# Optimization experiments

Hardware: AMD Instinct MI355X
Metric: run time of the kernel (lower is better)

## Reference

```python
import jax, jax.numpy as jnp
import numpy as np

B, N, D = 8, 2048, 512

def setup_inputs() -> dict:
    key = jax.random.key(0)
    ks = jax.random.split(key, 8)
    s = 1.0 / np.sqrt(D)
    return {
        "inputs": jax.random.normal(ks[0], (B, N, D), dtype=jnp.float32),
        "mask": jnp.ones((B, N), dtype=jnp.int32),
        "Wk": jax.random.normal(ks[1], (D, D), dtype=jnp.float32) * s,
        "bk": jax.random.normal(ks[2], (D,), dtype=jnp.float32) * s,
        "Wq": jax.random.normal(ks[3], (D, D), dtype=jnp.float32) * s,
        "bq": jax.random.normal(ks[4], (D,), dtype=jnp.float32) * s,
        "Wv": jax.random.normal(ks[5], (D, D), dtype=jnp.float32) * s,
        "bv": jax.random.normal(ks[6], (D,), dtype=jnp.float32) * s,
    }

def reference(inputs, mask, Wk, bk, Wq, bq, Wv, bv):
    # torch Linear: y = x @ W.T + b
    keys = jnp.einsum('bnd,ed->bne', inputs, Wk) + bk
    queries = jnp.einsum('bnd,ed->bne', inputs, Wq) + bq
    values = jnp.einsum('bnd,ed->bne', inputs, Wv) + bv
    norm = jnp.sqrt(jnp.asarray(D, inputs.dtype))
    scores = jnp.einsum('bqd,bkd->bqk', queries, keys) / norm  # [B,N,N]
    scores = jnp.where(mask[:, None, :] == 0, jnp.asarray(-1e9, scores.dtype), scores)
    attn = jax.nn.softmax(scores, axis=-1)
    return jnp.einsum('bqk,bkd->bqd', attn, values)
```

## Files before the change

### kernel.cpp

```cpp
#include <hip/hip_runtime.h>
#include <hip/hip_bf16.h>


typedef __attribute__((ext_vector_type(8))) short short8;
typedef __attribute__((ext_vector_type(4))) float f32x4;

#define DEV __device__ __forceinline__
#define GLOBAL_AS __attribute__((address_space(1)))
#define LDS_AS __attribute__((address_space(3)))

static DEV ushort f2bs(float f) {
  union { float f; unsigned u; } x; x.f = f;
  unsigned r = (x.u + 0x7fffu + ((x.u >> 16) & 1u)) >> 16;
  return (ushort)r;
}

static DEV f32x4 mfma16(short8 a, short8 b, f32x4 c) {
  return __builtin_amdgcn_mfma_f32_16x16x32_bf16(a, b, c, 0, 0, 0);
}

static DEV void async16(const void* g, void* l) {
  __builtin_amdgcn_global_load_lds((const GLOBAL_AS void*)g, (LDS_AS void*)l, 16, 0, 0);
}

__global__ void convert_all(const float* __restrict__ wq, const float* __restrict__ wk,
                            const float* __restrict__ wv, const float* __restrict__ x,
                            ushort* __restrict__ wb, ushort* __restrict__ xb,
                            float* __restrict__ lde) {
  int i = blockIdx.x * 256 + threadIdx.x;
  if (i >= 2293760) {
    int off = (i - 2293760) * 4;
    float4 z; z.x = 0.f; z.y = 0.f; z.z = 0.f; z.w = 0.f;
    *(float4*)(lde + off) = z;
    return;
  }
  const float* src;
  ushort* dst;
  if (i < 196608) {
    int which = i >> 16;
    int off = (i & 65535) * 4;
    src = ((which == 0) ? wq : (which == 1) ? wk : wv) + off;
    dst = wb + (size_t)which * 262144 + off;
  } else {
    int off = (i - 196608) * 4;
    src = x + off;
    dst = xb + off;
  }
  float4 v = *(const float4*)src;
  ushort4 o;
  o.x = f2bs(v.x); o.y = f2bs(v.y); o.z = f2bs(v.z); o.w = f2bs(v.w);
  *(ushort4*)dst = o;
}

#define KLOOP_STAGE(Aptr, lda, Bptr, ldb)                                      \
  do {                                                                         \
    _Pragma("unroll")                                                          \
    for (int t = 0; t < 8; t++) {                                              \
      int rowbase = (t & 3) * 32 + wave * 8;                                   \
      int r = rowbase + (lane >> 3);                                           \
      int gc = (lane & 7) ^ (r & 7);                                           \
      if (t < 4)                                                               \
        async16((Aptr) + (size_t)(rowblk * 128 + r) * (lda) + kb + gc * 8,     \
                &As[rowbase * 64]);                                            \
      else                                                                     \
        async16((Bptr) + (size_t)(colblk * 128 + r) * (ldb) + kb + gc * 8,     \
                &Bs[rowbase * 64]);                                            \
    }                                                                          \
  } while (0)

#define KLOOP_MFMA()                                                           \
  do {                                                                         \
    _Pragma("unroll")                                                          \
    for (int ks = 0; ks < 2; ks++) {                                           \
      short8 af[4], bfr[4];                                                    \
      _Pragma("unroll")                                                        \
      for (int t = 0; t < 4; t++) {                                            \
        int ra = wm * 64 + t * 16 + c16;                                       \
        int rb = wn * 64 + t * 16 + c16;                                       \
        af[t]  = *(const short8*)&As[ra * 64 + (((ks * 4 + quad) ^ (ra & 7)) * 8)]; \
        bfr[t] = *(const short8*)&Bs[rb * 64 + (((ks * 4 + quad) ^ (rb & 7)) * 8)]; \
      }                                                                        \
      _Pragma("unroll")                                                        \
      for (int mt = 0; mt < 4; mt++)                                           \
        _Pragma("unroll")                                                      \
        for (int nt = 0; nt < 4; nt++)                                         \
          acc[mt][nt] = mfma16(af[mt], bfr[nt], acc[mt][nt]);                  \
    }                                                                          \
  } while (0)

__launch_bounds__(256, 4)
__global__ void qkv_gemm(const ushort* __restrict__ Xb, const ushort* __restrict__ Wb,
                         const float* __restrict__ bq, const float* __restrict__ bk,
                         const float* __restrict__ bv,
                         ushort* __restrict__ Qb, ushort* __restrict__ Kb,
                         ushort* __restrict__ Vtb) {
  const int rowblk = blockIdx.x;
  const int colblk = blockIdx.y;
  const int z = colblk >> 2;

  __shared__ ushort S[2 * 128 * 64];
  ushort* As = S;
  ushort* Bs = S + 128 * 64;

  const int tid = threadIdx.x;
  const int wave = tid >> 6, lane = tid & 63, quad = lane >> 4, c16 = lane & 15;
  const int wm = wave & 1, wn = wave >> 1;

  f32x4 acc[4][4];
#pragma unroll
  for (int mt = 0; mt < 4; mt++)
#pragma unroll
    for (int nt = 0; nt < 4; nt++) acc[mt][nt] = (f32x4)0.0f;

  for (int kb = 0; kb < 512; kb += 64) {
    __syncthreads();
    KLOOP_STAGE(Xb, 512, Wb, 512);
    __syncthreads();
    KLOOP_MFMA();
  }

  const float* bias = (z == 0) ? bq : (z == 1) ? bk : bv;
  float bvals[4];
#pragma unroll
  for (int nt = 0; nt < 4; nt++) {
    int eg = colblk * 128 + wn * 64 + nt * 16 + c16;
    bvals[nt] = bias[eg & 511];
  }
  const float sc = (z == 0) ? 0.044194173824159216f : 1.0f;

  const int row0 = rowblk * 128 + wm * 64;
  const int col0 = colblk * 128 + wn * 64;
  if (z < 2) {
    ushort* O = (z == 0) ? Qb : Kb;
#pragma unroll
    for (int mt = 0; mt < 4; mt++)
#pragma unroll
      for (int nt = 0; nt < 4; nt++) {
        int el = (col0 + nt * 16 + c16) & 511;
#pragma unroll
        for (int r = 0; r < 4; r++) {
          int n = row0 + mt * 16 + quad * 4 + r;
          O[(size_t)n * 512 + el] = f2bs((acc[mt][nt][r] + bvals[nt]) * sc);
        }
      }
  } else {
    __syncthreads();
    ushort* T = S;
#pragma unroll
    for (int nt = 0; nt < 4; nt++) {
      int ell = wn * 64 + nt * 16 + c16;
#pragma unroll
      for (int mt = 0; mt < 4; mt++) {
        int n0l = wm * 64 + mt * 16 + quad * 4;
        ushort4 o;
        o.x = f2bs(acc[mt][nt][0] + bvals[nt]);
        o.y = f2bs(acc[mt][nt][1] + bvals[nt]);
        o.z = f2bs(acc[mt][nt][2] + bvals[nt]);
        o.w = f2bs(acc[mt][nt][3] + bvals[nt]);
        *(ushort4*)&T[ell * 128 + (((n0l >> 3) ^ (ell & 15)) << 3) + (n0l & 4)] = o;
      }
    }
    __syncthreads();
    const int c4 = tid & 3, er = tid >> 2;
    const int bb = rowblk >> 4;
    const int nbase = (rowblk & 15) * 128;
    const int elbase = (colblk & 3) * 128;
#pragma unroll
    for (int part = 0; part < 2; part++) {
      int ell = part * 64 + er;
      size_t ge = ((size_t)bb * 512 + elbase + ell) * 2048;
#pragma unroll
      for (int j2 = 0; j2 < 4; j2++) {
        int n0 = j2 * 32 + c4 * 8;
        short8 v = *(short8*)&T[ell * 128 + (((n0 >> 3) ^ (ell & 15)) << 3)];
        *(short8*)(Vtb + ge + nbase + n0) = v;
      }
    }
  }
}

__launch_bounds__(256, 4)
__global__ void gemm_s(const ushort* __restrict__ Kb, const ushort* __restrict__ Qb,
                       const int* __restrict__ mask, ushort* __restrict__ Pm,
                       float* __restrict__ l) {
  const int b = blockIdx.z;
  const int rowblk = blockIdx.x;
  const int colblk = blockIdx.y;
  const ushort* A  = Kb + (size_t)b * 2048 * 512;
  const ushort* Bq = Qb + (size_t)b * 2048 * 512;

  __shared__ ushort S[2 * 128 * 64];
  ushort* As = S;
  ushort* Bs = S + 128 * 64;

  const int tid = threadIdx.x;
  const int wave = tid >> 6, lane = tid & 63, quad = lane >> 4, c16 = lane & 15;
  const int wm = wave & 1, wn = wave >> 1;

  f32x4 acc[4][4];
#pragma unroll
  for (int mt = 0; mt < 4; mt++)
#pragma unroll
    for (int nt = 0; nt < 4; nt++) acc[mt][nt] = (f32x4)0.0f;

  for (int kb = 0; kb < 512; kb += 64) {
    __syncthreads();
    KLOOP_STAGE(A, 512, Bq, 512);
    __syncthreads();
    KLOOP_MFMA();
  }

  const int row0 = rowblk * 128 + wm * 64;
  const int col0 = colblk * 128 + wn * 64;
  float lpart[4] = {0.0f, 0.0f, 0.0f, 0.0f};

  __syncthreads();
  ushort* T = S;
#pragma unroll
  for (int mt = 0; mt < 4; mt++) {
    int key0 = row0 + mt * 16 + quad * 4;
    int k0l  = wm * 64 + mt * 16 + quad * 4;
    int4 mv = *(const int4*)&mask[b * 2048 + key0];
    float mf0 = mv.x ? 1.0f : 0.0f, mf1 = mv.y ? 1.0f : 0.0f;
    float mf2 = mv.z ? 1.0f : 0.0f, mf3 = mv.w ? 1.0f : 0.0f;
#pragma unroll
    for (int nt = 0; nt < 4; nt++) {
      int ql = wn * 64 + nt * 16 + c16;
      float p0 = __expf(acc[mt][nt][0]) * mf0;
      float p1 = __expf(acc[mt][nt][1]) * mf1;
      float p2 = __expf(acc[mt][nt][2]) * mf2;
      float p3 = __expf(acc[mt][nt][3]) * mf3;
      ushort4 o;
      o.x = f2bs(p0); o.y = f2bs(p1); o.z = f2bs(p2); o.w = f2bs(p3);
      *(ushort4*)&T[ql * 128 + (((k0l >> 3) ^ (ql & 15)) << 3) + (k0l & 4)] = o;
      lpart[nt] += p0 + p1 + p2 + p3;
    }
  }
#pragma unroll
  for (int nt = 0; nt < 4; nt++) {
    float v = lpart[nt];
    v += __shfl_xor(v, 16, 64);
    v += __shfl_xor(v, 32, 64);
    if (quad == 0) atomicAdd(&l[b * 2048 + col0 + nt * 16 + c16], v);
  }
  __syncthreads();
  {
    const int c4 = tid & 3, er = tid >> 2;
#pragma unroll
    for (int part = 0; part < 2; part++) {
      int ql = part * 64 + er;
      size_t gq = ((size_t)b * 2048 + colblk * 128 + ql) * 2048;
#pragma unroll
      for (int j2 = 0; j2 < 4; j2++) {
        int n0 = j2 * 32 + c4 * 8;
        short8 v = *(short8*)&T[ql * 128 + (((n0 >> 3) ^ (ql & 15)) << 3)];
        *(short8*)(Pm + gq + rowblk * 128 + n0) = v;
      }
    }
  }
}

__launch_bounds__(256, 4)
__global__ void gemm_o(const ushort* __restrict__ Pm, const ushort* __restrict__ Vtb,
                       const float* __restrict__ l, float* __restrict__ out) {
  const int b = blockIdx.z;
  const int rowblk = blockIdx.x;
  const int colblk = blockIdx.y;
  const ushort* A  = Pm  + (size_t)b * 2048 * 2048;
  const ushort* Bv = Vtb + (size_t)b * 512 * 2048;

  __shared__ ushort S[2 * 128 * 64];
  ushort* As = S;
  ushort* Bs = S + 128 * 64;

  const int tid = threadIdx.x;
  const int wave = tid >> 6, lane = tid & 63, quad = lane >> 4, c16 = lane & 15;
  const int wm = wave & 1, wn = wave >> 1;

  f32x4 acc[4][4];
#pragma unroll
  for (int mt = 0; mt < 4; mt++)
#pragma unroll
    for (int nt = 0; nt < 4; nt++) acc[mt][nt] = (f32x4)0.0f;

  for (int kb = 0; kb < 2048; kb += 64) {
    __syncthreads();
    KLOOP_STAGE(A, 2048, Bv, 2048);
    __syncthreads();
    KLOOP_MFMA();
  }

  const int row0 = rowblk * 128 + wm * 64;
  const int col0 = colblk * 128 + wn * 64;
  float linv[4][4];
#pragma unroll
  for (int mt = 0; mt < 4; mt++)
#pragma unroll
    for (int r = 0; r < 4; r++)
      linv[mt][r] = 1.0f / l[b * 2048 + row0 + mt * 16 + quad * 4 + r];
#pragma unroll
  for (int mt = 0; mt < 4; mt++)
#pragma unroll
    for (int nt = 0; nt < 4; nt++) {
      int col = col0 + nt * 16 + c16;
#pragma unroll
      for (int r = 0; r < 4; r++) {
        int row = row0 + mt * 16 + quad * 4 + r;
        out[((size_t)b * 2048 + row) * 512 + col] = acc[mt][nt][r] * linv[mt][r];
      }
    }
}

extern "C" void kernel_launch(void* const* d_in, const int* in_sizes, int n_in,
                              void* d_out, int out_size, void* d_ws, size_t ws_size,
                              hipStream_t stream) {
  (void)in_sizes; (void)n_in; (void)out_size; (void)ws_size;
  const float* X    = (const float*)d_in[0];
  const int*   mask = (const int*)d_in[1];
  const float* Wk   = (const float*)d_in[2];
  const float* bk   = (const float*)d_in[3];
  const float* Wq   = (const float*)d_in[4];
  const float* bq   = (const float*)d_in[5];
  const float* Wv   = (const float*)d_in[6];
  const float* bv   = (const float*)d_in[7];
  float* out = (float*)d_out;

  ushort* ws  = (ushort*)d_ws;
  ushort* Pm  = ws;
  ushort* Xb  = ws;
  ushort* Wb  = ws + (size_t)33554432;
  ushort* Qb  = Wb + (size_t)786432;
  ushort* Kb  = Qb + (size_t)8388608;
  ushort* Vtb = Kb + (size_t)8388608;
  float*  lde = (float*)(Vtb + (size_t)8388608);

  convert_all<<<8976, 256, 0, stream>>>(Wq, Wk, Wv, X, Wb, Xb, lde);
  qkv_gemm<<<dim3(128, 12), 256, 0, stream>>>(Xb, Wb, bq, bk, bv, Qb, Kb, Vtb);
  gemm_s<<<dim3(16, 16, 8), 256, 0, stream>>>(Kb, Qb, mask, Pm, lde);
  gemm_o<<<dim3(16, 4, 8), 256, 0, stream>>>(Pm, Vtb, lde, out);
}
```

Baseline: 217.2 us.

## Fuse score and output GEMMs into a single flash-style attention kernel

Replaces the separate score GEMM, which wrote the full bf16 probability matrix to global memory, and the output GEMM with one fused kernel. Each block keeps a 64-query tile resident in LDS and streams K and V tiles, holding exp scores in LDS. Row sums are accumulated in LDS rather than with global atomics, so the zeroing of the global sum buffer goes away. This removes the large Pm write and read, but the grid shrinks to 256 blocks of 512 threads with about 112KB of LDS each. K/V loads are not double-buffered, so occupancy is low and loads are exposed behind syncthreads.

```diff
diff --git a/kernel.cpp b/kernel.cpp
--- a/kernel.cpp
+++ b/kernel.cpp
@@ -25,15 +25,8 @@
 
 __global__ void convert_all(const float* __restrict__ wq, const float* __restrict__ wk,
                             const float* __restrict__ wv, const float* __restrict__ x,
-                            ushort* __restrict__ wb, ushort* __restrict__ xb,
-                            float* __restrict__ lde) {
+                            ushort* __restrict__ wb, ushort* __restrict__ xb) {
   int i = blockIdx.x * 256 + threadIdx.x;
-  if (i >= 2293760) {
-    int off = (i - 2293760) * 4;
-    float4 z; z.x = 0.f; z.y = 0.f; z.z = 0.f; z.w = 0.f;
-    *(float4*)(lde + off) = z;
-    return;
-  }
   const float* src;
   ushort* dst;
   if (i < 196608) {
@@ -179,134 +172,155 @@
   }
 }
 
-__launch_bounds__(256, 4)
-__global__ void gemm_s(const ushort* __restrict__ Kb, const ushort* __restrict__ Qb,
-                       const int* __restrict__ mask, ushort* __restrict__ Pm,
-                       float* __restrict__ l) {
-  const int b = blockIdx.z;
-  const int rowblk = blockIdx.x;
-  const int colblk = blockIdx.y;
-  const ushort* A  = Kb + (size_t)b * 2048 * 512;
-  const ushort* Bq = Qb + (size_t)b * 2048 * 512;
-
-  __shared__ ushort S[2 * 128 * 64];
-  ushort* As = S;
-  ushort* Bs = S + 128 * 64;
+__launch_bounds__(512, 2)
+__global__ void attn_fused(const ushort* __restrict__ Qb, const ushort* __restrict__ Kb,
+                           const ushort* __restrict__ Vtb, const int* __restrict__ mask,
+                           float* __restrict__ out) {
+  const int bid = blockIdx.x;
+  const int b = bid & 7;
+  const int qblk = bid >> 3;
+  const ushort* Qp = Qb + ((size_t)b * 2048 + qblk * 64) * 512;
+  const ushort* Kp = Kb + (size_t)b * 2048 * 512;
+  const ushort* Vp = Vtb + (size_t)b * 512 * 2048;
+
+  extern __shared__ ushort S[];
+  ushort* Qs  = S;
+  ushort* KVs = S + 32768;
+  ushort* Ps  = S + 49152;
+  float*  l_lds = (float*)(S + 57344);
 
   const int tid = threadIdx.x;
   const int wave = tid >> 6, lane = tid & 63, quad = lane >> 4, c16 = lane & 15;
-  const int wm = wave & 1, wn = wave >> 1;
-
-  f32x4 acc[4][4];
-#pragma unroll
-  for (int mt = 0; mt < 4; mt++)
-#pragma unroll
-    for (int nt = 0; nt < 4; nt++) acc[mt][nt] = (f32x4)0.0f;
-
-  for (int kb = 0; kb < 512; kb += 64) {
-    __syncthreads();
-    KLOOP_STAGE(A, 512, Bq, 512);
-    __syncthreads();
-    KLOOP_MFMA();
-  }
-
-  const int row0 = rowblk * 128 + wm * 64;
-  const int col0 = colblk * 128 + wn * 64;
-  float lpart[4] = {0.0f, 0.0f, 0.0f, 0.0f};
-
-  __syncthreads();
-  ushort* T = S;
-#pragma unroll
-  for (int mt = 0; mt < 4; mt++) {
-    int key0 = row0 + mt * 16 + quad * 4;
-    int k0l  = wm * 64 + mt * 16 + quad * 4;
-    int4 mv = *(const int4*)&mask[b * 2048 + key0];
-    float mf0 = mv.x ? 1.0f : 0.0f, mf1 = mv.y ? 1.0f : 0.0f;
-    float mf2 = mv.z ? 1.0f : 0.0f, mf3 = mv.w ? 1.0f : 0.0f;
-#pragma unroll
-    for (int nt = 0; nt < 4; nt++) {
-      int ql = wn * 64 + nt * 16 + c16;
-      float p0 = __expf(acc[mt][nt][0]) * mf0;
-      float p1 = __expf(acc[mt][nt][1]) * mf1;
-      float p2 = __expf(acc[mt][nt][2]) * mf2;
-      float p3 = __expf(acc[mt][nt][3]) * mf3;
-      ushort4 o;
-      o.x = f2bs(p0); o.y = f2bs(p1); o.z = f2bs(p2); o.w = f2bs(p3);
-      *(ushort4*)&T[ql * 128 + (((k0l >> 3) ^ (ql & 15)) << 3) + (k0l & 4)] = o;
-      lpart[nt] += p0 + p1 + p2 + p3;
-    }
-  }
-#pragma unroll
-  for (int nt = 0; nt < 4; nt++) {
+  const int wk = wave & 3, wq = wave >> 2;
+  const int wq2 = wave & 1, wd = wave >> 1;
+
+  if (tid < 64) l_lds[tid] = 0.0f;
+
+#pragma unroll
+  for (int i = 0; i < 8; i++) {
+    int r = wave * 8 + i;
+    int gc = (lane & 48) | ((lane & 15) ^ (r & 15));
+    async16(Qp + (size_t)r * 512 + gc * 8, &Qs[r * 512]);
+  }
+
+  f32x4 acc_o[2][8];
+#pragma unroll
+  for (int mt = 0; mt < 2; mt++)
+#pragma unroll
+    for (int j = 0; j < 8; j++) acc_o[mt][j] = (f32x4)0.0f;
+  float lpart[2] = {0.0f, 0.0f};
+
+  for (int kt = 0; kt < 16; kt++) {
+    const int key0 = kt * 128;
+    f32x4 acc_s[2][2];
+#pragma unroll
+    for (int mt = 0; mt < 2; mt++)
+#pragma unroll
+      for (int nt = 0; nt < 2; nt++) acc_s[mt][nt] = (f32x4)0.0f;
+
+    for (int dc = 0; dc < 4; dc++) {
+      __syncthreads();
+#pragma unroll
+      for (int t = 0; t < 4; t++) {
+        int rowbase = t * 32 + wave * 4;
+        int r = rowbase + (lane >> 4);
+        int gc = (lane & 15) ^ (r & 15);
+        async16(Kp + (size_t)(key0 + r) * 512 + dc * 128 + gc * 8, &KVs[rowbase * 128]);
+      }
+      __syncthreads();
+#pragma unroll
+      for (int ks = 0; ks < 4; ks++) {
+        short8 af[2], qf[2];
+#pragma unroll
+        for (int t = 0; t < 2; t++) {
+          int rk = wk * 32 + t * 16 + c16;
+          af[t] = *(const short8*)&KVs[rk * 128 + (((ks * 4 + quad) ^ (rk & 15)) * 8)];
+          int rq = wq * 32 + t * 16 + c16;
+          int cg = dc * 16 + ks * 4 + quad;
+          qf[t] = *(const short8*)&Qs[rq * 512 + (((cg & 48) | ((cg & 15) ^ (rq & 15))) * 8)];
+        }
+#pragma unroll
+        for (int mt = 0; mt < 2; mt++)
+#pragma unroll
+          for (int nt = 0; nt < 2; nt++)
+            acc_s[mt][nt] = mfma16(af[mt], qf[nt], acc_s[mt][nt]);
+      }
+    }
+
+#pragma unroll
+    for (int mt = 0; mt < 2; mt++) {
+      int k0l = wk * 32 + mt * 16 + quad * 4;
+      int4 mv = *(const int4*)&mask[b * 2048 + key0 + k0l];
+      float mf0 = mv.x ? 1.0f : 0.0f, mf1 = mv.y ? 1.0f : 0.0f;
+      float mf2 = mv.z ? 1.0f : 0.0f, mf3 = mv.w ? 1.0f : 0.0f;
+#pragma unroll
+      for (int nt = 0; nt < 2; nt++) {
+        int ql = wq * 32 + nt * 16 + c16;
+        float p0 = __expf(acc_s[mt][nt][0]) * mf0;
+        float p1 = __expf(acc_s[mt][nt][1]) * mf1;
+        float p2 = __expf(acc_s[mt][nt][2]) * mf2;
+        float p3 = __expf(acc_s[mt][nt][3]) * mf3;
+        ushort4 o;
+        o.x = f2bs(p0); o.y = f2bs(p1); o.z = f2bs(p2); o.w = f2bs(p3);
+        *(ushort4*)&Ps[ql * 128 + (((k0l >> 3) ^ (ql & 15)) << 3) + (k0l & 4)] = o;
+        lpart[nt] += p0 + p1 + p2 + p3;
+      }
+    }
+
+#pragma unroll
+    for (int dv = 0; dv < 4; dv++) {
+      __syncthreads();
+#pragma unroll
+      for (int t = 0; t < 4; t++) {
+        int rowbase = t * 32 + wave * 4;
+        int r = rowbase + (lane >> 4);
+        int gc = (lane & 15) ^ (r & 15);
+        async16(Vp + (size_t)(dv * 128 + r) * 2048 + key0 + gc * 8, &KVs[rowbase * 128]);
+      }
+      __syncthreads();
+#pragma unroll
+      for (int ks = 0; ks < 4; ks++) {
+        short8 ap[2], vf[2];
+#pragma unroll
+        for (int t = 0; t < 2; t++) {
+          int rq = wq2 * 32 + t * 16 + c16;
+          ap[t] = *(const short8*)&Ps[rq * 128 + (((ks * 4 + quad) ^ (rq & 15)) * 8)];
+          int rd = wd * 32 + t * 16 + c16;
+          vf[t] = *(const short8*)&KVs[rd * 128 + (((ks * 4 + quad) ^ (rd & 15)) * 8)];
+        }
+#pragma unroll
+        for (int mt = 0; mt < 2; mt++)
+#pragma unroll
+          for (int nt = 0; nt < 2; nt++)
+            acc_o[mt][dv * 2 + nt] = mfma16(ap[mt], vf[nt], acc_o[mt][dv * 2 + nt]);
+      }
+    }
+  }
+
+#pragma unroll
+  for (int nt = 0; nt < 2; nt++) {
     float v = lpart[nt];
     v += __shfl_xor(v, 16, 64);
     v += __shfl_xor(v, 32, 64);
-    if (quad == 0) atomicAdd(&l[b * 2048 + col0 + nt * 16 + c16], v);
+    if (quad == 0) atomicAdd(&l_lds[wq * 32 + nt * 16 + c16], v);
   }
   __syncthreads();
-  {
-    const int c4 = tid & 3, er = tid >> 2;
-#pragma unroll
-    for (int part = 0; part < 2; part++) {
-      int ql = part * 64 + er;
-      size_t gq = ((size_t)b * 2048 + colblk * 128 + ql) * 2048;
-#pragma unroll
-      for (int j2 = 0; j2 < 4; j2++) {
-        int n0 = j2 * 32 + c4 * 8;
-        short8 v = *(short8*)&T[ql * 128 + (((n0 >> 3) ^ (ql & 15)) << 3)];
-        *(short8*)(Pm + gq + rowblk * 128 + n0) = v;
-      }
-    }
-  }
-}
-
-__launch_bounds__(256, 4)
-__global__ void gemm_o(const ushort* __restrict__ Pm, const ushort* __restrict__ Vtb,
-                       const float* __restrict__ l, float* __restrict__ out) {
-  const int b = blockIdx.z;
-  const int rowblk = blockIdx.x;
-  const int colblk = blockIdx.y;
-  const ushort* A  = Pm  + (size_t)b * 2048 * 2048;
-  const ushort* Bv = Vtb + (size_t)b * 512 * 2048;
-
-  __shared__ ushort S[2 * 128 * 64];
-  ushort* As = S;
-  ushort* Bs = S + 128 * 64;
-
-  const int tid = threadIdx.x;
-  const int wave = tid >> 6, lane = tid & 63, quad = lane >> 4, c16 = lane & 15;
-  const int wm = wave & 1, wn = wave >> 1;
-
-  f32x4 acc[4][4];
-#pragma unroll
-  for (int mt = 0; mt < 4; mt++)
-#pragma unroll
-    for (int nt = 0; nt < 4; nt++) acc[mt][nt] = (f32x4)0.0f;
-
-  for (int kb = 0; kb < 2048; kb += 64) {
-    __syncthreads();
-    KLOOP_STAGE(A, 2048, Bv, 2048);
-    __syncthreads();
-    KLOOP_MFMA();
-  }
-
-  const int row0 = rowblk * 128 + wm * 64;
-  const int col0 = colblk * 128 + wn * 64;
-  float linv[4][4];
-#pragma unroll
-  for (int mt = 0; mt < 4; mt++)
+
+  float linv[2][4];
+#pragma unroll
+  for (int mt = 0; mt < 2; mt++)
 #pragma unroll
     for (int r = 0; r < 4; r++)
-      linv[mt][r] = 1.0f / l[b * 2048 + row0 + mt * 16 + quad * 4 + r];
-#pragma unroll
-  for (int mt = 0; mt < 4; mt++)
-#pragma unroll
-    for (int nt = 0; nt < 4; nt++) {
-      int col = col0 + nt * 16 + c16;
+      linv[mt][r] = 1.0f / l_lds[wq2 * 32 + mt * 16 + quad * 4 + r];
+#pragma unroll
+  for (int mt = 0; mt < 2; mt++)
+#pragma unroll
+    for (int j = 0; j < 8; j++) {
+      int d = (j >> 1) * 128 + wd * 32 + (j & 1) * 16 + c16;
 #pragma unroll
       for (int r = 0; r < 4; r++) {
-        int row = row0 + mt * 16 + quad * 4 + r;
-        out[((size_t)b * 2048 + row) * 512 + col] = acc[mt][nt][r] * linv[mt][r];
+        int row = qblk * 64 + wq2 * 32 + mt * 16 + quad * 4 + r;
+        out[((size_t)b * 2048 + row) * 512 + d] = acc_o[mt][j][r] * linv[mt][r];
       }
     }
 }
@@ -326,16 +340,13 @@
   float* out = (float*)d_out;
 
   ushort* ws  = (ushort*)d_ws;
-  ushort* Pm  = ws;
   ushort* Xb  = ws;
-  ushort* Wb  = ws + (size_t)33554432;
+  ushort* Wb  = Xb + (size_t)8388608;
   ushort* Qb  = Wb + (size_t)786432;
   ushort* Kb  = Qb + (size_t)8388608;
   ushort* Vtb = Kb + (size_t)8388608;
-  float*  lde = (float*)(Vtb + (size_t)8388608);
-
-  convert_all<<<8976, 256, 0, stream>>>(Wq, Wk, Wv, X, Wb, Xb, lde);
+
+  convert_all<<<8960, 256, 0, stream>>>(Wq, Wk, Wv, X, Wb, Xb);
   qkv_gemm<<<dim3(128, 12), 256, 0, stream>>>(Xb, Wb, bq, bk, bv, Qb, Kb, Vtb);
-  gemm_s<<<dim3(16, 16, 8), 256, 0, stream>>>(Kb, Qb, mask, Pm, lde);
-  gemm_o<<<dim3(16, 4, 8), 256, 0, stream>>>(Pm, Vtb, lde, out);
-}
+  attn_fused<<<256, 512, 114944, stream>>>(Qb, Kb, Vtb, mask, out);
+}
```

After: 250.8 us. +15.4%, slower.

## Use 256x256 double-buffered tiles with 512 threads for QKV and score GEMMs

Applied to the files above, without the earlier changes.

Rewrites qkv_gemm and gemm_s to compute 256x256 output tiles with 8 waves, each wave owning 128x64 (32 MFMA accumulators). The K-loop prefetches two stages ahead into a double-buffered 128KB dynamic LDS region with explicit vmcnt waits and barriers, and raises wave priority around the MFMA bursts. This is meant to increase data reuse per loaded byte and overlap global loads with compute. In exchange it uses far more LDS and registers, allows fewer resident blocks, and launches fewer blocks (384 and 512) across the CUs.

```diff
diff --git a/kernel.cpp b/kernel.cpp
--- a/kernel.cpp
+++ b/kernel.cpp
@@ -52,6 +52,229 @@
   *(ushort4*)dst = o;
 }
 
+#define STAGE256(buf, Aptr, lda, Bptr, ldb, kb)                                \
+  do {                                                                         \
+    ushort* bA_ = Sd + (buf) * 32768;                                          \
+    ushort* bB_ = bA_ + 16384;                                                 \
+    _Pragma("unroll")                                                          \
+    for (int st = 0; st < 8; st++) {                                           \
+      int rowbase = (st & 3) * 64 + wave * 8;                                  \
+      int r = rowbase + (lane >> 3);                                           \
+      int gc = (lane & 7) ^ (r & 7);                                           \
+      if (st < 4)                                                              \
+        async16((Aptr) + (size_t)(rowblk * 256 + r) * (lda) + (kb) + gc * 8,   \
+                &bA_[rowbase * 64]);                                           \
+      else                                                                     \
+        async16((Bptr) + (size_t)(colblk * 256 + r) * (ldb) + (kb) + gc * 8,   \
+                &bB_[rowbase * 64]);                                           \
+    }                                                                          \
+  } while (0)
+
+#define COMPUTE256(buf)                                                        \
+  do {                                                                         \
+    const ushort* cA_ = Sd + (buf) * 32768;                                    \
+    const ushort* cB_ = cA_ + 16384;                                           \
+    _Pragma("unroll")                                                          \
+    for (int ks = 0; ks < 2; ks++) {                                           \
+      short8 af[8], bf[4];                                                     \
+      _Pragma("unroll")                                                        \
+      for (int mf = 0; mf < 8; mf++) {                                         \
+        int ra = wm * 128 + mf * 16 + c16;                                     \
+        af[mf] = *(const short8*)&cA_[ra * 64 + (((ks * 4 + quad) ^ (ra & 7)) * 8)]; \
+      }                                                                        \
+      _Pragma("unroll")                                                        \
+      for (int nf = 0; nf < 4; nf++) {                                         \
+        int rb = wn * 64 + nf * 16 + c16;                                      \
+        bf[nf] = *(const short8*)&cB_[rb * 64 + (((ks * 4 + quad) ^ (rb & 7)) * 8)]; \
+      }                                                                        \
+      __builtin_amdgcn_s_setprio(1);                                           \
+      _Pragma("unroll")                                                        \
+      for (int mf = 0; mf < 8; mf++)                                           \
+        _Pragma("unroll")                                                      \
+        for (int nf = 0; nf < 4; nf++)                                         \
+          acc[mf][nf] = mfma16(af[mf], bf[nf], acc[mf][nf]);                   \
+      __builtin_amdgcn_s_setprio(0);                                           \
+    }                                                                          \
+  } while (0)
+
+#define KLOOP256(Aptr, lda, Bptr, ldb, NT)                                     \
+  do {                                                                         \
+    STAGE256(0, Aptr, lda, Bptr, ldb, 0);                                      \
+    STAGE256(1, Aptr, lda, Bptr, ldb, 64);                                     \
+    asm volatile("s_waitcnt vmcnt(8)" ::: "memory");                           \
+    __builtin_amdgcn_sched_barrier(0);                                         \
+    __builtin_amdgcn_s_barrier();                                              \
+    __builtin_amdgcn_sched_barrier(0);                                         \
+    for (int t = 0; t < (NT); t++) {                                           \
+      COMPUTE256(t & 1);                                                       \
+      if (t == (NT) - 1) break;                                                \
+      __builtin_amdgcn_sched_barrier(0);                                       \
+      __builtin_amdgcn_s_barrier();                                            \
+      __builtin_amdgcn_sched_barrier(0);                                       \
+      if (t + 2 < (NT)) {                                                      \
+        STAGE256(t & 1, Aptr, lda, Bptr, ldb, (t + 2) * 64);                   \
+        asm volatile("s_waitcnt vmcnt(8)" ::: "memory");                       \
+      } else {                                                                 \
+        asm volatile("s_waitcnt vmcnt(0)" ::: "memory");                       \
+      }                                                                        \
+      __builtin_amdgcn_sched_barrier(0);                                       \
+      __builtin_amdgcn_s_barrier();                                            \
+      __builtin_amdgcn_sched_barrier(0);                                       \
+    }                                                                          \
+  } while (0)
+
+__launch_bounds__(512, 2)
+__global__ void qkv_gemm(const ushort* __restrict__ Xb, const ushort* __restrict__ Wb,
+                         const float* __restrict__ bq, const float* __restrict__ bk,
+                         const float* __restrict__ bv,
+                         ushort* __restrict__ Qb, ushort* __restrict__ Kb,
+                         ushort* __restrict__ Vtb) {
+  const int rowblk = blockIdx.x;
+  const int colblk = blockIdx.y;
+  const int z = colblk >> 1;
+
+  extern __shared__ ushort Sd[];
+
+  const int tid = threadIdx.x;
+  const int wave = tid >> 6, lane = tid & 63, quad = lane >> 4, c16 = lane & 15;
+  const int wm = wave >> 2, wn = wave & 3;
+
+  f32x4 acc[8][4];
+#pragma unroll
+  for (int mf = 0; mf < 8; mf++)
+#pragma unroll
+    for (int nf = 0; nf < 4; nf++) acc[mf][nf] = (f32x4)0.0f;
+
+  KLOOP256(Xb, 512, Wb, 512, 8);
+
+  const float* bias = (z == 0) ? bq : (z == 1) ? bk : bv;
+  float bvals[4];
+#pragma unroll
+  for (int nf = 0; nf < 4; nf++)
+    bvals[nf] = bias[(colblk & 1) * 256 + wn * 64 + nf * 16 + c16];
+  const float sc = (z == 0) ? 0.044194173824159216f : 1.0f;
+
+  const int row0 = rowblk * 256 + wm * 128;
+  if (z < 2) {
+    ushort* O = (z == 0) ? Qb : Kb;
+#pragma unroll
+    for (int mf = 0; mf < 8; mf++)
+#pragma unroll
+      for (int nf = 0; nf < 4; nf++) {
+        int el = (colblk & 1) * 256 + wn * 64 + nf * 16 + c16;
+#pragma unroll
+        for (int r = 0; r < 4; r++) {
+          int n = row0 + mf * 16 + quad * 4 + r;
+          O[(size_t)n * 512 + el] = f2bs((acc[mf][nf][r] + bvals[nf]) * sc);
+        }
+      }
+  } else {
+    __syncthreads();
+    ushort* T = Sd;
+#pragma unroll
+    for (int nf = 0; nf < 4; nf++) {
+      int ell = wn * 64 + nf * 16 + c16;
+#pragma unroll
+      for (int mf = 0; mf < 8; mf++) {
+        int n0 = wm * 128 + mf * 16 + quad * 4;
+        ushort4 o;
+        o.x = f2bs(acc[mf][nf][0] + bvals[nf]);
+        o.y = f2bs(acc[mf][nf][1] + bvals[nf]);
+        o.z = f2bs(acc[mf][nf][2] + bvals[nf]);
+        o.w = f2bs(acc[mf][nf][3] + bvals[nf]);
+        *(ushort4*)&T[ell * 256 + (((n0 >> 3) ^ (ell & 31)) << 3) + (n0 & 4)] = o;
+      }
+    }
+    __syncthreads();
+    const int b = rowblk >> 3;
+    const int nbase = (rowblk & 7) * 256;
+    const int elbase = (colblk & 1) * 256;
+    const int c4 = tid & 3;
+#pragma unroll
+    for (int outer = 0; outer < 2; outer++) {
+      int er = outer * 128 + (tid >> 2);
+      size_t ge = ((size_t)b * 512 + elbase + er) * 2048;
+#pragma unroll
+      for (int j = 0; j < 8; j++) {
+        int ch = j * 4 + c4;
+        short8 v = *(short8*)&T[er * 256 + ((ch ^ (er & 31)) << 3)];
+        *(short8*)(Vtb + ge + nbase + ch * 8) = v;
+      }
+    }
+  }
+}
+
+__launch_bounds__(512, 2)
+__global__ void gemm_s(const ushort* __restrict__ Kb, const ushort* __restrict__ Qb,
+                       const int* __restrict__ mask, ushort* __restrict__ Pm,
+                       float* __restrict__ l) {
+  const int b = blockIdx.z;
+  const int rowblk = blockIdx.x;
+  const int colblk = blockIdx.y;
+  const ushort* A  = Kb + (size_t)b * 2048 * 512;
+  const ushort* Bq = Qb + (size_t)b * 2048 * 512;
+
+  extern __shared__ ushort Sd[];
+
+  const int tid = threadIdx.x;
+  const int wave = tid >> 6, lane = tid & 63, quad = lane >> 4, c16 = lane & 15;
+  const int wm = wave >> 2, wn = wave & 3;
+
+  f32x4 acc[8][4];
+#pragma unroll
+  for (int mf = 0; mf < 8; mf++)
+#pragma unroll
+    for (int nf = 0; nf < 4; nf++) acc[mf][nf] = (f32x4)0.0f;
+
+  KLOOP256(A, 512, Bq, 512, 8);
+
+  float lpart[4] = {0.0f, 0.0f, 0.0f, 0.0f};
+  __syncthreads();
+  ushort* T = Sd;
+#pragma unroll
+  for (int mf = 0; mf < 8; mf++) {
+    int keyl = wm * 128 + mf * 16 + quad * 4;
+    int4 mv = *(const int4*)&mask[b * 2048 + rowblk * 256 + keyl];
+    float m0 = mv.x ? 1.0f : 0.0f, m1 = mv.y ? 1.0f : 0.0f;
+    float m2 = mv.z ? 1.0f : 0.0f, m3 = mv.w ? 1.0f : 0.0f;
+#pragma unroll
+    for (int nf = 0; nf < 4; nf++) {
+      int ql = wn * 64 + nf * 16 + c16;
+      float p0 = __expf(acc[mf][nf][0]) * m0;
+      float p1 = __expf(acc[mf][nf][1]) * m1;
+      float p2 = __expf(acc[mf][nf][2]) * m2;
+      float p3 = __expf(acc[mf][nf][3]) * m3;
+      ushort4 o;
+      o.x = f2bs(p0); o.y = f2bs(p1); o.z = f2bs(p2); o.w = f2bs(p3);
+      *(ushort4*)&T[ql * 256 + (((keyl >> 3) ^ (ql & 31)) << 3) + (keyl & 4)] = o;
+      lpart[nf] += p0 + p1 + p2 + p3;
+    }
+  }
+#pragma unroll
+  for (int nf = 0; nf < 4; nf++) {
+    float v = lpart[nf];
+    v += __shfl_xor(v, 16, 64);
+    v += __shfl_xor(v, 32, 64);
+    if (quad == 0)
+      atomicAdd(&l[b * 2048 + colblk * 256 + wn * 64 + nf * 16 + c16], v);
+  }
+  __syncthreads();
+  {
+    const int c4 = tid & 3;
+#pragma unroll
+    for (int outer = 0; outer < 2; outer++) {
+      int qr = outer * 128 + (tid >> 2);
+      size_t gq = ((size_t)b * 2048 + colblk * 256 + qr) * 2048;
+#pragma unroll
+      for (int j = 0; j < 8; j++) {
+        int ch = j * 4 + c4;
+        short8 v = *(short8*)&T[qr * 256 + ((ch ^ (qr & 31)) << 3)];
+        *(short8*)(Pm + gq + rowblk * 256 + ch * 8) = v;
+      }
+    }
+  }
+}
+
 #define KLOOP_STAGE(Aptr, lda, Bptr, ldb)                                      \
   do {                                                                         \
     _Pragma("unroll")                                                          \
@@ -87,178 +310,6 @@
           acc[mt][nt] = mfma16(af[mt], bfr[nt], acc[mt][nt]);                  \
     }                                                                          \
   } while (0)
-
-__launch_bounds__(256, 4)
-__global__ void qkv_gemm(const ushort* __restrict__ Xb, const ushort* __restrict__ Wb,
-                         const float* __restrict__ bq, const float* __restrict__ bk,
-                         const float* __restrict__ bv,
-                         ushort* __restrict__ Qb, ushort* __restrict__ Kb,
-                         ushort* __restrict__ Vtb) {
-  const int rowblk = blockIdx.x;
-  const int colblk = blockIdx.y;
-  const int z = colblk >> 2;
-
-  __shared__ ushort S[2 * 128 * 64];
-  ushort* As = S;
-  ushort* Bs = S + 128 * 64;
-
-  const int tid = threadIdx.x;
-  const int wave = tid >> 6, lane = tid & 63, quad = lane >> 4, c16 = lane & 15;
-  const int wm = wave & 1, wn = wave >> 1;
-
-  f32x4 acc[4][4];
-#pragma unroll
-  for (int mt = 0; mt < 4; mt++)
-#pragma unroll
-    for (int nt = 0; nt < 4; nt++) acc[mt][nt] = (f32x4)0.0f;
-
-  for (int kb = 0; kb < 512; kb += 64) {
-    __syncthreads();
-    KLOOP_STAGE(Xb, 512, Wb, 512);
-    __syncthreads();
-    KLOOP_MFMA();
-  }
-
-  const float* bias = (z == 0) ? bq : (z == 1) ? bk : bv;
-  float bvals[4];
-#pragma unroll
-  for (int nt = 0; nt < 4; nt++) {
-    int eg = colblk * 128 + wn * 64 + nt * 16 + c16;
-    bvals[nt] = bias[eg & 511];
-  }
-  const float sc = (z == 0) ? 0.044194173824159216f : 1.0f;
-
-  const int row0 = rowblk * 128 + wm * 64;
-  const int col0 = colblk * 128 + wn * 64;
-  if (z < 2) {
-    ushort* O = (z == 0) ? Qb : Kb;
-#pragma unroll
-    for (int mt = 0; mt < 4; mt++)
-#pragma unroll
-      for (int nt = 0; nt < 4; nt++) {
-        int el = (col0 + nt * 16 + c16) & 511;
-#pragma unroll
-        for (int r = 0; r < 4; r++) {
-          int n = row0 + mt * 16 + quad * 4 + r;
-          O[(size_t)n * 512 + el] = f2bs((acc[mt][nt][r] + bvals[nt]) * sc);
-        }
-      }
-  } else {
-    __syncthreads();
-    ushort* T = S;
-#pragma unroll
-    for (int nt = 0; nt < 4; nt++) {
-      int ell = wn * 64 + nt * 16 + c16;
-#pragma unroll
-      for (int mt = 0; mt < 4; mt++) {
-        int n0l = wm * 64 + mt * 16 + quad * 4;
-        ushort4 o;
-        o.x = f2bs(acc[mt][nt][0] + bvals[nt]);
-        o.y = f2bs(acc[mt][nt][1] + bvals[nt]);
-        o.z = f2bs(acc[mt][nt][2] + bvals[nt]);
-        o.w = f2bs(acc[mt][nt][3] + bvals[nt]);
-        *(ushort4*)&T[ell * 128 + (((n0l >> 3) ^ (ell & 15)) << 3) + (n0l & 4)] = o;
-      }
-    }
-    __syncthreads();
-    const int c4 = tid & 3, er = tid >> 2;
-    const int bb = rowblk >> 4;
-    const int nbase = (rowblk & 15) * 128;
-    const int elbase = (colblk & 3) * 128;
-#pragma unroll
-    for (int part = 0; part < 2; part++) {
-      int ell = part * 64 + er;
-      size_t ge = ((size_t)bb * 512 + elbase + ell) * 2048;
-#pragma unroll
-      for (int j2 = 0; j2 < 4; j2++) {
-        int n0 = j2 * 32 + c4 * 8;
-        short8 v = *(short8*)&T[ell * 128 + (((n0 >> 3) ^ (ell & 15)) << 3)];
-        *(short8*)(Vtb + ge + nbase + n0) = v;
-      }
-    }
-  }
-}
-
-__launch_bounds__(256, 4)
-__global__ void gemm_s(const ushort* __restrict__ Kb, const ushort* __restrict__ Qb,
-                       const int* __restrict__ mask, ushort* __restrict__ Pm,
-                       float* __restrict__ l) {
-  const int b = blockIdx.z;
-  const int rowblk = blockIdx.x;
-  const int colblk = blockIdx.y;
-  const ushort* A  = Kb + (size_t)b * 2048 * 512;
-  const ushort* Bq = Qb + (size_t)b * 2048 * 512;
-
-  __shared__ ushort S[2 * 128 * 64];
-  ushort* As = S;
-  ushort* Bs = S + 128 * 64;
-
-  const int tid = threadIdx.x;
-  const int wave = tid >> 6, lane = tid & 63, quad = lane >> 4, c16 = lane & 15;
-  const int wm = wave & 1, wn = wave >> 1;
-
-  f32x4 acc[4][4];
-#pragma unroll
-  for (int mt = 0; mt < 4; mt++)
-#pragma unroll
-    for (int nt = 0; nt < 4; nt++) acc[mt][nt] = (f32x4)0.0f;
-
-  for (int kb = 0; kb < 512; kb += 64) {
-    __syncthreads();
-    KLOOP_STAGE(A, 512, Bq, 512);
-    __syncthreads();
-    KLOOP_MFMA();
-  }
-
-  const int row0 = rowblk * 128 + wm * 64;
-  const int col0 = colblk * 128 + wn * 64;
-  float lpart[4] = {0.0f, 0.0f, 0.0f, 0.0f};
-
-  __syncthreads();
-  ushort* T = S;
-#pragma unroll
-  for (int mt = 0; mt < 4; mt++) {
-    int key0 = row0 + mt * 16 + quad * 4;
-    int k0l  = wm * 64 + mt * 16 + quad * 4;
-    int4 mv = *(const int4*)&mask[b * 2048 + key0];
-    float mf0 = mv.x ? 1.0f : 0.0f, mf1 = mv.y ? 1.0f : 0.0f;
-    float mf2 = mv.z ? 1.0f : 0.0f, mf3 = mv.w ? 1.0f : 0.0f;
-#pragma unroll
-    for (int nt = 0; nt < 4; nt++) {
-      int ql = wn * 64 + nt * 16 + c16;
-      float p0 = __expf(acc[mt][nt][0]) * mf0;
-      float p1 = __expf(acc[mt][nt][1]) * mf1;
-      float p2 = __expf(acc[mt][nt][2]) * mf2;
-      float p3 = __expf(acc[mt][nt][3]) * mf3;
-      ushort4 o;
-      o.x = f2bs(p0); o.y = f2bs(p1); o.z = f2bs(p2); o.w = f2bs(p3);
-      *(ushort4*)&T[ql * 128 + (((k0l >> 3) ^ (ql & 15)) << 3) + (k0l & 4)] = o;
-      lpart[nt] += p0 + p1 + p2 + p3;
-    }
-  }
-#pragma unroll
-  for (int nt = 0; nt < 4; nt++) {
-    float v = lpart[nt];
-    v += __shfl_xor(v, 16, 64);
-    v += __shfl_xor(v, 32, 64);
-    if (quad == 0) atomicAdd(&l[b * 2048 + col0 + nt * 16 + c16], v);
-  }
-  __syncthreads();
-  {
-    const int c4 = tid & 3, er = tid >> 2;
-#pragma unroll
-    for (int part = 0; part < 2; part++) {
-      int ql = part * 64 + er;
-      size_t gq = ((size_t)b * 2048 + colblk * 128 + ql) * 2048;
-#pragma unroll
-      for (int j2 = 0; j2 < 4; j2++) {
-        int n0 = j2 * 32 + c4 * 8;
-        short8 v = *(short8*)&T[ql * 128 + (((n0 >> 3) ^ (ql & 15)) << 3)];
-        *(short8*)(Pm + gq + rowblk * 128 + n0) = v;
-      }
-    }
-  }
-}
 
 __launch_bounds__(256, 4)
 __global__ void gemm_o(const ushort* __restrict__ Pm, const ushort* __restrict__ Vtb,
@@ -335,7 +386,7 @@
   float*  lde = (float*)(Vtb + (size_t)8388608);
 
   convert_all<<<8976, 256, 0, stream>>>(Wq, Wk, Wv, X, Wb, Xb, lde);
-  qkv_gemm<<<dim3(128, 12), 256, 0, stream>>>(Xb, Wb, bq, bk, bv, Qb, Kb, Vtb);
-  gemm_s<<<dim3(16, 16, 8), 256, 0, stream>>>(Kb, Qb, mask, Pm, lde);
+  qkv_gemm<<<dim3(64, 6), 512, 131072, stream>>>(Xb, Wb, bq, bk, bv, Qb, Kb, Vtb);
+  gemm_s<<<dim3(8, 8, 8), 512, 131072, stream>>>(Kb, Qb, mask, Pm, lde);
   gemm_o<<<dim3(16, 4, 8), 256, 0, stream>>>(Pm, Vtb, lde, out);
 }
```

New measurement: 224.0 us. 3.1% more time.

## Rewrite P·V GEMM as 256x128-tile, 8-wave, double-buffered async pipeline

Applied to the files above, without the earlier changes.

The output GEMM (P times V) now runs 512-thread blocks, each computing a 256x128 tile. Operand tiles are loaded with async global-to-LDS copies into a double-buffered, XOR-swizzled dynamic shared buffer. The next tile's loads are interleaved with the current tile's MFMA phases, using explicit waitcnt and barriers plus s_setprio around MFMAs. This hides load latency and improves operand reuse, in exchange for 96KB of LDS per block, lower occupancy and fragile hand-scheduled synchronisation. Blocks are remapped to a 1D grid with batch as the fastest-varying index.

```diff
diff --git a/kernel.cpp b/kernel.cpp
--- a/kernel.cpp
+++ b/kernel.cpp
@@ -260,53 +260,134 @@
   }
 }
 
-__launch_bounds__(256, 4)
+#define OST_A(pp, kt, rd)                                                      \
+  do {                                                                         \
+    int rowbase_ = (rd) * 64 + wave * 8;                                       \
+    int r_ = rowbase_ + (lane >> 3);                                           \
+    int gc_ = (lane & 7) ^ (r_ & 7);                                           \
+    async16(A + (size_t)(rowblk * 256 + r_) * 2048 + (kt) * 64 + gc_ * 8,      \
+            SdA + (pp) * 16384 + rowbase_ * 64);                               \
+  } while (0)
+
+#define OST_B(pp, kt, rd)                                                      \
+  do {                                                                         \
+    int rowbase_ = (rd) * 64 + wave * 8;                                       \
+    int r_ = rowbase_ + (lane >> 3);                                           \
+    int gc_ = (lane & 7) ^ (r_ & 7);                                           \
+    async16(Bv + (size_t)(colblk * 128 + r_) * 2048 + (kt) * 64 + gc_ * 8,     \
+            SdB + (pp) * 8192 + rowbase_ * 64);                                \
+  } while (0)
+
+#define OREAD(pp, ks, afx, bfx)                                                \
+  do {                                                                         \
+    const ushort* Ap_ = SdA + (pp) * 16384;                                    \
+    const ushort* Bp_ = SdB + (pp) * 8192;                                     \
+    _Pragma("unroll")                                                          \
+    for (int mf = 0; mf < 4; mf++) {                                           \
+      int ra = wm * 64 + mf * 16 + c16;                                        \
+      afx[mf] = *(const short8*)&Ap_[ra * 64 + ((((ks)*4 + quad) ^ (ra & 7)) * 8)]; \
+    }                                                                          \
+    _Pragma("unroll")                                                          \
+    for (int nf = 0; nf < 4; nf++) {                                           \
+      int rb = wn * 64 + nf * 16 + c16;                                        \
+      bfx[nf] = *(const short8*)&Bp_[rb * 64 + ((((ks)*4 + quad) ^ (rb & 7)) * 8)]; \
+    }                                                                          \
+  } while (0)
+
+#define OMFMA(afx, bfx, h)                                                     \
+  do {                                                                         \
+    __builtin_amdgcn_s_setprio(1);                                             \
+    _Pragma("unroll")                                                          \
+    for (int mf = (h) * 2; mf < (h) * 2 + 2; mf++)                             \
+      _Pragma("unroll")                                                        \
+      for (int nf = 0; nf < 4; nf++)                                           \
+        acc[mf][nf] = mfma16(afx[mf], bfx[nf], acc[mf][nf]);                   \
+    __builtin_amdgcn_s_setprio(0);                                             \
+  } while (0)
+
+#define OTILE(pp, kt, dostage)                                                 \
+  do {                                                                         \
+    OREAD(pp, 0, af0, bf0);                                                    \
+    __builtin_amdgcn_s_barrier();                                              \
+    asm volatile("s_waitcnt lgkmcnt(0)" ::: "memory");                         \
+    __builtin_amdgcn_sched_barrier(0);                                         \
+    OMFMA(af0, bf0, 0);                                                        \
+    __builtin_amdgcn_s_barrier();                                              \
+    OREAD(pp, 1, af1, bf1);                                                    \
+    __builtin_amdgcn_s_barrier();                                              \
+    asm volatile("s_waitcnt lgkmcnt(0)" ::: "memory");                         \
+    __builtin_amdgcn_sched_barrier(0);                                         \
+    OMFMA(af0, bf0, 1);                                                        \
+    __builtin_amdgcn_s_barrier();         \
+    if (dostage) { OST_A(pp, (kt) + 2, 0); OST_A(pp, (kt) + 2, 1);             \
+                   OST_A(pp, (kt) + 2, 2); }                                   \
+    OMFMA(af1, bf1, 0);                                                        \
+    __builtin_amdgcn_s_barrier();                                              \
+    if (dostage) { OST_A(pp, (kt) + 2, 3); OST_B(pp, (kt) + 2, 0);             \
+                   OST_B(pp, (kt) + 2, 1); }                                   \
+    OMFMA(af1, bf1, 1);                                                        \
+    if (dostage) { asm volatile("s_waitcnt vmcnt(6)" ::: "memory"); }          \
+    else         { asm volatile("s_waitcnt vmcnt(0)" ::: "memory"); }          \
+    __builtin_amdgcn_sched_barrier(0);                                         \
+    __builtin_amdgcn_s_barrier();        \
+  } while (0)
+
+__launch_bounds__(512, 2)
 __global__ void gemm_o(const ushort* __restrict__ Pm, const ushort* __restrict__ Vtb,
                        const float* __restrict__ l, float* __restrict__ out) {
-  const int b = blockIdx.z;
-  const int rowblk = blockIdx.x;
-  const int colblk = blockIdx.y;
+  const int bid = blockIdx.x;
+  const int b = bid & 7;
+  const int rowblk = (bid >> 3) & 7;
+  const int colblk = bid >> 6;
   const ushort* A  = Pm  + (size_t)b * 2048 * 2048;
   const ushort* Bv = Vtb + (size_t)b * 512 * 2048;
 
-  __shared__ ushort S[2 * 128 * 64];
-  ushort* As = S;
-  ushort* Bs = S + 128 * 64;
+  extern __shared__ ushort Sd[];
+  ushort* SdA = Sd;
+  ushort* SdB = Sd + 32768;
 
   const int tid = threadIdx.x;
   const int wave = tid >> 6, lane = tid & 63, quad = lane >> 4, c16 = lane & 15;
-  const int wm = wave & 1, wn = wave >> 1;
+  const int wm = wave >> 1, wn = wave & 1;
 
   f32x4 acc[4][4];
 #pragma unroll
-  for (int mt = 0; mt < 4; mt++)
-#pragma unroll
-    for (int nt = 0; nt < 4; nt++) acc[mt][nt] = (f32x4)0.0f;
-
-  for (int kb = 0; kb < 2048; kb += 64) {
-    __syncthreads();
-    KLOOP_STAGE(A, 2048, Bv, 2048);
-    __syncthreads();
-    KLOOP_MFMA();
-  }
-
-  const int row0 = rowblk * 128 + wm * 64;
+  for (int mf = 0; mf < 4; mf++)
+#pragma unroll
+    for (int nf = 0; nf < 4; nf++) acc[mf][nf] = (f32x4)0.0f;
+
+  OST_A(0, 0, 0); OST_A(0, 0, 1); OST_A(0, 0, 2); OST_A(0, 0, 3);
+  OST_B(0, 0, 0); OST_B(0, 0, 1);
+  OST_A(1, 1, 0); OST_A(1, 1, 1); OST_A(1, 1, 2); OST_A(1, 1, 3);
+  OST_B(1, 1, 0); OST_B(1, 1, 1);
+  asm volatile("s_waitcnt vmcnt(6)" ::: "memory");
+  __builtin_amdgcn_sched_barrier(0);
+  __builtin_amdgcn_s_barrier();
+
+  short8 af0[4], bf0[4], af1[4], bf1[4];
+  for (int i = 0; i < 16; i++) {
+    const int dostage = (i < 15);
+    OTILE(0, 2 * i, dostage);
+    OTILE(1, 2 * i + 1, dostage);
+  }
+
+  const int row0 = rowblk * 256 + wm * 64;
   const int col0 = colblk * 128 + wn * 64;
   float linv[4][4];
 #pragma unroll
-  for (int mt = 0; mt < 4; mt++)
+  for (int mf = 0; mf < 4; mf++)
 #pragma unroll
     for (int r = 0; r < 4; r++)
-      linv[mt][r] = 1.0f / l[b * 2048 + row0 + mt * 16 + quad * 4 + r];
-#pragma unroll
-  for (int mt = 0; mt < 4; mt++)
-#pragma unroll
-    for (int nt = 0; nt < 4; nt++) {
-      int col = col0 + nt * 16 + c16;
+      linv[mf][r] = 1.0f / l[b * 2048 + row0 + mf * 16 + quad * 4 + r];
+#pragma unroll
+  for (int mf = 0; mf < 4; mf++)
+#pragma unroll
+    for (int nf = 0; nf < 4; nf++) {
+      int col = col0 + nf * 16 + c16;
 #pragma unroll
       for (int r = 0; r < 4; r++) {
-        int row = row0 + mt * 16 + quad * 4 + r;
-        out[((size_t)b * 2048 + row) * 512 + col] = acc[mt][nt][r] * linv[mt][r];
+        int row = row0 + mf * 16 + quad * 4 + r;
+        out[((size_t)b * 2048 + row) * 512 + col] = acc[mf][nf][r] * linv[mf][r];
       }
     }
 }
@@ -337,5 +418,5 @@
   convert_all<<<8976, 256, 0, stream>>>(Wq, Wk, Wv, X, Wb, Xb, lde);
   qkv_gemm<<<dim3(128, 12), 256, 0, stream>>>(Xb, Wb, bq, bk, bv, Qb, Kb, Vtb);
   gemm_s<<<dim3(16, 16, 8), 256, 0, stream>>>(Kb, Qb, mask, Pm, lde);
-  gemm_o<<<dim3(16, 4, 8), 256, 0, stream>>>(Pm, Vtb, lde, out);
-}
+  gemm_o<<<256, 512, 98304, stream>>>(Pm, Vtb, lde, out);
+}
```

Measured after the change: 204.7 us. -5.8%, faster.
